# Performance work log

Measured on AMD Instinct MI355X. Metric: run time of the kernel, lower is better.

The kernel has to match this reference:

```python
import jax, jax.numpy as jnp
import numpy as np

N = 1_000_000
H, W = 480, 640
MIN_DEPTH, MAX_DEPTH = 0.0, 30.0


def setup_inputs() -> dict:
    key = jax.random.key(0)
    k1, k2, k3 = jax.random.split(key, 3)
    scale = jnp.array([W - 1, H - 1], dtype=jnp.float32)
    mkpts0_f = jax.random.uniform(k1, (N, 2), dtype=jnp.float32) * scale
    mkpts1_f = jax.random.uniform(k2, (N, 2), dtype=jnp.float32) * scale
    mconf = jax.random.uniform(k3, (N,), dtype=jnp.float32)
    K = jnp.array([[520.0, 0.0, 320.0],
                   [0.0, 520.0, 240.0],
                   [0.0, 0.0, 1.0]], dtype=jnp.float32)
    K0 = K[None]  # [1,3,3]
    K1 = K[None]
    c, s = float(np.cos(0.1)), float(np.sin(0.1))
    T_0to1 = jnp.array([[c, 0.0, s, 0.2],
                        [0.0, 1.0, 0.0, 0.0],
                        [-s, 0.0, c, 0.05],
                        [0.0, 0.0, 0.0, 1.0]], dtype=jnp.float32)[None]  # [1,4,4]
    image0 = jnp.zeros((1, 1, H, W), dtype=jnp.float32)
    m_bids = jnp.zeros((N,), dtype=jnp.int32)  # single batch element
    return {"T_0to1": T_0to1, "K0": K0, "K1": K1, "mconf": mconf,
            "mkpts0_f": mkpts0_f, "mkpts1_f": mkpts1_f,
            "image0": image0, "m_bids": m_bids}


def _triangulate(T_0to1, K0, K1, mconf, kpts0, kpts1):
    # Projection matrices: P0 = K0 @ [I|0], P1 = K1 @ T[:3,:]
    proj_identity = jnp.eye(3, 4, dtype=K0.dtype)
    P0 = K0[0] @ proj_identity          # [3,4]
    P1 = K1[0] @ T_0to1[0, :3, :]       # [3,4]
    P = jnp.stack([P0, P1], axis=0)     # [V=2,3,4]

    pts = jnp.stack([kpts0, kpts1], axis=1)              # [N,2,2]
    conf = jnp.stack([jnp.ones_like(mconf), mconf], 1)   # [N,2] (self conf = 1)

    # A[n,v] = pts[n,v,:,None] * P[v,2,None,:] - P[v,:2]   -> [N,V,2,4]
    A = pts[..., None] * P[None, :, 2, None, :] - P[None, :, :2, :]
    A = A * conf[:, :, None, None]
    A = A.reshape(A.shape[0], 4, 4)                       # [N,4,4]

    # torch.svd returns V with A = U S V^T; jnp gives Vh = V^T.
    _, _, Vh = jnp.linalg.svd(A)
    v = -Vh[:, 3, :]                                      # [N,4] = -V[:,:,3]
    points_3d = v[:, :3] / v[:, 3:4]                      # homogeneous -> euclidean
    # torch clamps to [-1000,1000] only when infs appear; the final depth value
    # after [0,30] clamp + filter is identical either way, so clip unconditionally.
    points_3d = jnp.clip(points_3d, -1000.0, 1000.0)

    z = jnp.clip(points_3d[:, 2], MIN_DEPTH, MAX_DEPTH)
    filt = (z > MIN_DEPTH) & (z < MAX_DEPTH)
    kp3d_val = z * filt.astype(z.dtype)
    return kp3d_val, points_3d


def reference(T_0to1, K0, K1, mconf, mkpts0_f, mkpts1_f, image0, m_bids):
    h, w = image0.shape[-2], image0.shape[-1]
    kp3d_val, _ = _triangulate(T_0to1, K0, K1, mconf, mkpts0_f, mkpts1_f)
    # generate_sparse_depth: depth[0, y, x] = kp3d_val (long() truncation)
    xi = mkpts0_f[:, 0].astype(jnp.int32)
    yi = mkpts0_f[:, 1].astype(jnp.int32)
    depth0_sparse = jnp.zeros((1, h, w), dtype=kp3d_val.dtype).at[0, yi, xi].set(kp3d_val)
    return depth0_sparse, kp3d_val
```

## Files before the change

### kernel.cpp

```cpp
#include <hip/hip_runtime.h>
#include <math.h>

#define N_PTS 1000000
#define H_IMG 480
#define W_IMG 640
#define PIX (H_IMG * W_IMG)
#define TPB 256
#define BPTS 1024
#define NBLK ((N_PTS + BPTS - 1) / BPTS)


__device__ __forceinline__ double frcp1(double b) {
  double r = __builtin_amdgcn_rcp(b);
  r = fma(fma(-b, r, 1.0), r, r);
  return r;
}
__device__ __forceinline__ double frcp2(double b) {
  double r = __builtin_amdgcn_rcp(b);
  r = fma(fma(-b, r, 1.0), r, r);
  r = fma(fma(-b, r, 1.0), r, r);
  return r;
}
__device__ __forceinline__ double fsqrt_pos(double x) {
  double r = __builtin_amdgcn_rsq(x);
  double y = x * r;
  return fma(0.5 * r, fma(-y, y, x), y);
}

#define ROT64(p, q)                                                            \
  do {                                                                         \
    double apq = Mv[p][q];                                                     \
    if (apq != 0.0) {                                                          \
      double app = Mv[p][p], aqq = Mv[q][q];                                   \
      double d = aqq - app;                                                    \
      double r = sqrt(fma(d, d, 4.0 * apq * apq));                             \
      double t = (2.0 * apq) / (d + copysign(r, d));                           \
      double c = rsqrt(fma(t, t, 1.0));                                        \
      double s = t * c;                                                        \
      Mv[p][p] = fma(-t, apq, app);                                            \
      Mv[q][q] = fma(t, apq, aqq);                                             \
      Mv[p][q] = 0.0;                                                          \
      Mv[q][p] = 0.0;                                                          \
      _Pragma("unroll") for (int k = 0; k < 4; k++) {                          \
        if (k != p && k != q) {                                                \
          double akp = Mv[k][p], akq = Mv[k][q];                               \
          double nkp = c * akp - s * akq;                                      \
          double nkq = s * akp + c * akq;                                      \
          Mv[k][p] = nkp; Mv[p][k] = nkp;                                      \
          Mv[k][q] = nkq; Mv[q][k] = nkq;                                      \
        }                                                                      \
      }                                                                        \
      { double v2p = Vr2[p], v2q = Vr2[q];                                     \
        Vr2[p] = c * v2p - s * v2q; Vr2[q] = s * v2p + c * v2q; }              \
      { double v3p = Vr3[p], v3q = Vr3[q];                                     \
        Vr3[p] = c * v3p - s * v3q; Vr3[q] = s * v3p + c * v3q; }              \
    }                                                                          \
  } while (0)

__device__ float tri_point_fp64(int n,
                                const float* __restrict__ T,
                                const float* __restrict__ K0,
                                const float* __restrict__ K1,
                                const float* __restrict__ mconf,
                                const float* __restrict__ kp0,
                                const float* __restrict__ kp1) {
  float2 p0 = ((const float2*)kp0)[n];
  float2 p1 = ((const float2*)kp1)[n];
  double conf = (double)mconf[n];
  double x0 = (double)p0.x, y0 = (double)p0.y;
  double x1 = (double)p1.x, y1 = (double)p1.y;

  double P0[3][4];
#pragma unroll
  for (int i = 0; i < 3; i++) {
#pragma unroll
    for (int j = 0; j < 3; j++) P0[i][j] = (double)K0[i * 3 + j];
    P0[i][3] = 0.0;
  }
  double P1[3][4];
#pragma unroll
  for (int i = 0; i < 3; i++) {
#pragma unroll
    for (int j = 0; j < 4; j++) {
      double s = 0.0;
#pragma unroll
      for (int k = 0; k < 3; k++)
        s += (double)K1[i * 3 + k] * (double)T[k * 4 + j];
      P1[i][j] = s;
    }
  }

  double Mv[4][4];
#pragma unroll
  for (int i = 0; i < 4; i++)
#pragma unroll
    for (int j = 0; j < 4; j++) Mv[i][j] = 0.0;

  double a[4];
#pragma unroll
  for (int j = 0; j < 4; j++) a[j] = x0 * P0[2][j] - P0[0][j];
#pragma unroll
  for (int i = 0; i < 4; i++)
#pragma unroll
    for (int j = 0; j < 4; j++) Mv[i][j] = fma(a[i], a[j], Mv[i][j]);
#pragma unroll
  for (int j = 0; j < 4; j++) a[j] = y0 * P0[2][j] - P0[1][j];
#pragma unroll
  for (int i = 0; i < 4; i++)
#pragma unroll
    for (int j = 0; j < 4; j++) Mv[i][j] = fma(a[i], a[j], Mv[i][j]);
#pragma unroll
  for (int j = 0; j < 4; j++) a[j] = conf * (x1 * P1[2][j] - P1[0][j]);
#pragma unroll
  for (int i = 0; i < 4; i++)
#pragma unroll
    for (int j = 0; j < 4; j++) Mv[i][j] = fma(a[i], a[j], Mv[i][j]);
#pragma unroll
  for (int j = 0; j < 4; j++) a[j] = conf * (y1 * P1[2][j] - P1[1][j]);
#pragma unroll
  for (int i = 0; i < 4; i++)
#pragma unroll
    for (int j = 0; j < 4; j++) Mv[i][j] = fma(a[i], a[j], Mv[i][j]);

  double Vr2[4] = {0.0, 0.0, 1.0, 0.0};
  double Vr3[4] = {0.0, 0.0, 0.0, 1.0};

  for (int sweep = 0; sweep < 4; sweep++) {
    ROT64(0, 1); ROT64(0, 2); ROT64(0, 3);
    ROT64(1, 2); ROT64(1, 3); ROT64(2, 3);
  }

  double e0 = Mv[0][0], e1 = Mv[1][1], e2 = Mv[2][2], e3 = Mv[3][3];
  bool b01 = e1 < e0;
  double ea = b01 ? e1 : e0;
  double za = b01 ? Vr2[1] : Vr2[0];
  double wa = b01 ? Vr3[1] : Vr3[0];
  bool b23 = e3 < e2;
  double eb = b23 ? e3 : e2;
  double zb = b23 ? Vr2[3] : Vr2[2];
  double wb = b23 ? Vr3[3] : Vr3[2];
  bool bf = eb < ea;
  double vz = bf ? zb : za;
  double vw = bf ? wb : wa;

  double z = vz / vw;
  z = fmin(fmax(z, 0.0), 30.0);
  bool filt = (z > 0.0) && (z < 30.0);
  return filt ? (float)z : 0.0f;
}

struct G10 { double m00, m01, m02, m03, m11, m12, m13, m22, m23, m33; };
struct P4 { double t1, t2, t3, t4; };
struct Adj10 { double a00, a01, a02, a03, a11, a12, a13, a22, a23, a33; };

__device__ __forceinline__ G10 gram(float2 p0, float2 p1, float conff,
                                    const double (&P0d)[3][4],
                                    const double (&P1d)[3][4]) {
  G10 g;
  g.m00 = g.m01 = g.m02 = g.m03 = g.m11 = 0.0;
  g.m12 = g.m13 = g.m22 = g.m23 = g.m33 = 0.0;
  double x0 = (double)p0.x, y0 = (double)p0.y;
  double x1 = (double)p1.x, y1 = (double)p1.y;
  double cf = (double)conff;
  double a[4];
#pragma unroll
  for (int rr = 0; rr < 4; rr++) {
    if (rr == 0) {
#pragma unroll
      for (int j = 0; j < 4; j++) a[j] = fma(x0, P0d[2][j], -P0d[0][j]);
    } else if (rr == 1) {
#pragma unroll
      for (int j = 0; j < 4; j++) a[j] = fma(y0, P0d[2][j], -P0d[1][j]);
    } else if (rr == 2) {
#pragma unroll
      for (int j = 0; j < 4; j++) a[j] = cf * fma(x1, P1d[2][j], -P1d[0][j]);
    } else {
#pragma unroll
      for (int j = 0; j < 4; j++) a[j] = cf * fma(y1, P1d[2][j], -P1d[1][j]);
    }
    g.m00 = fma(a[0], a[0], g.m00); g.m01 = fma(a[0], a[1], g.m01);
    g.m02 = fma(a[0], a[2], g.m02); g.m03 = fma(a[0], a[3], g.m03);
    g.m11 = fma(a[1], a[1], g.m11); g.m12 = fma(a[1], a[2], g.m12);
    g.m13 = fma(a[1], a[3], g.m13); g.m22 = fma(a[2], a[2], g.m22);
    g.m23 = fma(a[2], a[3], g.m23); g.m33 = fma(a[3], a[3], g.m33);
  }
  return g;
}

__device__ __forceinline__ P4 charpoly(const G10& m) {
  P4 p;
  p.t1 = (m.m00 + m.m11) + (m.m22 + m.m33);
  double ms0 = fma(m.m00, m.m11, -m.m01 * m.m01);
  double ms1 = fma(m.m00, m.m12, -m.m02 * m.m01);
  double ms2 = fma(m.m00, m.m13, -m.m03 * m.m01);
  double ms3 = fma(m.m01, m.m12, -m.m02 * m.m11);
  double ms4 = fma(m.m01, m.m13, -m.m03 * m.m11);
  double mc0 = fma(m.m02, m.m13, -m.m12 * m.m03);
  double mc1 = fma(m.m02, m.m23, -m.m22 * m.m03);
  double mc2 = fma(m.m02, m.m33, -m.m23 * m.m03);
  double mc3 = fma(m.m12, m.m23, -m.m22 * m.m13);
  double mc4 = fma(m.m12, m.m33, -m.m23 * m.m13);
  double mc5 = fma(m.m22, m.m33, -m.m23 * m.m23);
  double A00 = fma(m.m11, mc5, fma(-m.m12, mc4, m.m13 * mc3));
  double A01 = -fma(m.m01, mc5, fma(-m.m02, mc4, m.m03 * mc3));
  double A11 = fma(m.m00, mc5, fma(-m.m02, mc2, m.m03 * mc1));
  double A02 = fma(m.m01, mc4, fma(-m.m11, mc2, m.m13 * mc0));
  double A03 = -fma(m.m01, mc3, fma(-m.m11, mc1, m.m12 * mc0));
  double A22 = fma(m.m03, ms4, fma(-m.m13, ms2, m.m33 * ms0));
  double A33 = fma(m.m02, ms3, fma(-m.m12, ms1, m.m22 * ms0));
  p.t3 = (A00 + A11) + (A22 + A33);
  p.t4 = fma(m.m00, A00, fma(m.m01, A01, fma(m.m02, A02, m.m03 * A03)));
  double q02 = fma(m.m00, m.m22, -m.m02 * m.m02);
  double q03 = fma(m.m00, m.m33, -m.m03 * m.m03);
  double q12 = fma(m.m11, m.m22, -m.m12 * m.m12);
  double q13 = fma(m.m11, m.m33, -m.m13 * m.m13);
  p.t2 = ((ms0 + mc5) + (q02 + q03)) + (q12 + q13);
  return p;
}

__device__ __forceinline__ double lag_step(const P4& p, double mu,
                                           double t1_3, double t1_6,
                                           double t2_2) {
  double pv = fma(fma(fma(mu - p.t1, mu, p.t2), mu, -p.t3), mu, p.t4);
  double pd = fma(fma(fma(4.0, mu, -t1_3), mu, t2_2), mu, -p.t3);
  double pdd = fma(fma(12.0, mu, -t1_6), mu, t2_2);
  double rad = 3.0 * fma(3.0 * pd, pd, -4.0 * pv * pdd);
  double sq = fsqrt_pos(fmax(rad, 1e-300));
  double den = pd + copysign(sq, pd);
  return fma(-4.0 * pv, frcp1(den), mu);
}

__device__ __forceinline__ Adj10 adjugate(const G10& m, double mu) {
  double b00 = m.m00 - mu, b11 = m.m11 - mu;
  double b22 = m.m22 - mu, b33 = m.m33 - mu;
  double s0 = fma(b00, b11, -m.m01 * m.m01);
  double s1 = fma(b00, m.m12, -m.m02 * m.m01);
  double s2 = fma(b00, m.m13, -m.m03 * m.m01);
  double s3 = fma(m.m01, m.m12, -m.m02 * b11);
  double s4 = fma(m.m01, m.m13, -m.m03 * b11);
  double c0 = fma(m.m02, m.m13, -m.m12 * m.m03);
  double c1 = fma(m.m02, m.m23, -b22 * m.m03);
  double c2 = fma(m.m02, b33, -m.m23 * m.m03);
  double c3 = fma(m.m12, m.m23, -b22 * m.m13);
  double c4 = fma(m.m12, b33, -m.m23 * m.m13);
  double c5 = fma(b22, b33, -m.m23 * m.m23);
  Adj10 A;
  A.a00 = fma(b11, c5, fma(-m.m12, c4, m.m13 * c3));
  A.a01 = -fma(m.m01, c5, fma(-m.m02, c4, m.m03 * c3));
  A.a11 = fma(b00, c5, fma(-m.m02, c2, m.m03 * c1));
  A.a02 = fma(m.m01, c4, fma(-b11, c2, m.m13 * c0));
  A.a12 = -fma(b00, c4, fma(-m.m01, c2, m.m03 * c0));
  A.a22 = fma(m.m03, s4, fma(-m.m13, s2, b33 * s0));
  A.a03 = -fma(m.m01, c3, fma(-b11, c1, m.m12 * c0));
  A.a13 = fma(b00, c3, fma(-m.m01, c1, m.m02 * c0));
  A.a23 = -fma(m.m03, s3, fma(-m.m13, s1, m.m23 * s0));
  A.a33 = fma(m.m02, s3, fma(-m.m12, s1, b22 * s0));
  return A;
}

__device__ __forceinline__ void finish(const Adj10& A, double* z_out,
                                       bool* ok_out) {
  double w10 = A.a00, w11 = A.a01, w12 = A.a02, w13 = A.a03;
  double bd = fabs(A.a00);
  { double d1 = fabs(A.a11);
    bool c = d1 > bd;
    w10 = c ? A.a01 : w10; w11 = c ? A.a11 : w11;
    w12 = c ? A.a12 : w12; w13 = c ? A.a13 : w13; bd = c ? d1 : bd; }
  { double d2 = fabs(A.a22);
    bool c = d2 > bd;
    w10 = c ? A.a02 : w10; w11 = c ? A.a12 : w11;
    w12 = c ? A.a22 : w12; w13 = c ? A.a23 : w13; bd = c ? d2 : bd; }
  { double d3 = fabs(A.a33);
    bool c = d3 > bd;
    w10 = c ? A.a03 : w10; w11 = c ? A.a13 : w11;
    w12 = c ? A.a23 : w12; w13 = c ? A.a33 : w13; }

  double u0 = fma(A.a00, w10, fma(A.a01, w11, fma(A.a02, w12, A.a03 * w13)));
  double u1 = fma(A.a01, w10, fma(A.a11, w11, fma(A.a12, w12, A.a13 * w13)));
  double u2 = fma(A.a02, w10, fma(A.a12, w11, fma(A.a22, w12, A.a23 * w13)));
  double u3 = fma(A.a03, w10, fma(A.a13, w11, fma(A.a23, w12, A.a33 * w13)));
  double v2 = fma(A.a02, u0, fma(A.a12, u1, fma(A.a22, u2, A.a23 * u3)));
  double v3 = fma(A.a03, u0, fma(A.a13, u1, fma(A.a23, u2, A.a33 * u3)));

  double z3 = v2 * frcp2(v3);

  double cross = fabs(fma(v2, u3, -(u2 * v3)));
  double rhs = 1e-3 * fmax(fabs(v3 * u3), fabs(v2 * u3));
  *ok_out = (cross < rhs) && (fabs(z3 - 30.0) > 0.1);
  *z_out = z3;
}

__global__ __launch_bounds__(TPB, 2) void tri_main(
    const float* __restrict__ T,
    const float* __restrict__ K0,
    const float* __restrict__ K1,
    const float* __restrict__ mconf,
    const float* __restrict__ kp0,
    const float* __restrict__ kp1,
    float* __restrict__ out_kp3d,
    unsigned long long* __restrict__ ws_pix)
{
  __shared__ unsigned short s_list[BPTS];
  __shared__ int s_cnt;

  int tid = threadIdx.x;
  int base = blockIdx.x * BPTS;
  if (tid == 0) s_cnt = 0;
  __syncthreads();

  double P0d[3][4], P1d[3][4];
#pragma unroll
  for (int i = 0; i < 3; i++) {
#pragma unroll
    for (int j = 0; j < 3; j++) P0d[i][j] = (double)K0[i * 3 + j];
    P0d[i][3] = 0.0;
  }
#pragma unroll
  for (int i = 0; i < 3; i++) {
#pragma unroll
    for (int j = 0; j < 4; j++) {
      double s = 0.0;
#pragma unroll
      for (int k = 0; k < 3; k++)
        s += (double)K1[i * 3 + k] * (double)T[k * 4 + j];
      P1d[i][j] = s;
    }
  }

#pragma unroll 1
  for (int r = 0; r < BPTS / (2 * TPB); r++) {
    int l0 = r * (2 * TPB) + tid;
    int l1 = l0 + TPB;
    int n0 = base + l0;
    int n1 = base + l1;
    bool act0 = n0 < N_PTS;
    bool act1 = n1 < N_PTS;
    int nc0 = act0 ? n0 : (N_PTS - 1);
    int nc1 = act1 ? n1 : (N_PTS - 1);

    float2 p0a = ((const float2*)kp0)[nc0];
    float2 p1a = ((const float2*)kp1)[nc0];
    float cfa = mconf[nc0];
    float2 p0b = ((const float2*)kp0)[nc1];
    float2 p1b = ((const float2*)kp1)[nc1];
    float cfb = mconf[nc1];

    G10 gA = gram(p0a, p1a, cfa, P0d, P1d);
    G10 gB = gram(p0b, p1b, cfb, P0d, P1d);
    P4 cA = charpoly(gA);
    P4 cB = charpoly(gB);
    double muA = cA.t4 * frcp1(cA.t3);
    double muB = cB.t4 * frcp1(cB.t3);
    double t1_3A = 3.0 * cA.t1, t1_6A = 6.0 * cA.t1, t2_2A = 2.0 * cA.t2;
    double t1_3B = 3.0 * cB.t1, t1_6B = 6.0 * cB.t1, t2_2B = 2.0 * cB.t2;
#pragma unroll
    for (int it = 0; it < 3; it++) {
      muA = lag_step(cA, muA, t1_3A, t1_6A, t2_2A);
      muB = lag_step(cB, muB, t1_3B, t1_6B, t2_2B);
    }
    Adj10 aA = adjugate(gA, muA);
    Adj10 aB = adjugate(gB, muB);
    double zA, zB;
    bool okA, okB;
    finish(aA, &zA, &okA);
    finish(aB, &zB, &okB);

    if (act0) {
      if (okA) {
        double zc = fmin(fmax(zA, 0.0), 30.0);
        bool filt = (zc > 0.0) && (zc < 30.0);
        float kp = filt ? (float)zc : 0.0f;
        out_kp3d[n0] = kp;
        int pix = (int)p0a.y * W_IMG + (int)p0a.x;
        atomicMax(&ws_pix[pix],
                  ((unsigned long long)(0xC0000000u | (unsigned)n0) << 32) |
                      (unsigned long long)__float_as_uint(kp));
      } else {
        int idx = atomicAdd(&s_cnt, 1);
        s_list[idx] = (unsigned short)l0;
      }
    }
    if (act1) {
      if (okB) {
        double zc = fmin(fmax(zB, 0.0), 30.0);
        bool filt = (zc > 0.0) && (zc < 30.0);
        float kp = filt ? (float)zc : 0.0f;
        out_kp3d[n1] = kp;
        int pix = (int)p0b.y * W_IMG + (int)p0b.x;
        atomicMax(&ws_pix[pix],
                  ((unsigned long long)(0xC0000000u | (unsigned)n1) << 32) |
                      (unsigned long long)__float_as_uint(kp));
      } else {
        int idx = atomicAdd(&s_cnt, 1);
        s_list[idx] = (unsigned short)l1;
      }
    }
  }

  __syncthreads();

  int cnt = s_cnt;
  for (int i = tid; i < cnt; i += TPB) {
    int n = base + (int)s_list[i];
    float kp = tri_point_fp64(n, T, K0, K1, mconf, kp0, kp1);
    out_kp3d[n] = kp;
    float2 p0 = ((const float2*)kp0)[n];
    int pix = (int)p0.y * W_IMG + (int)p0.x;
    atomicMax(&ws_pix[pix],
              ((unsigned long long)(0xC0000000u | (unsigned)n) << 32) |
                  (unsigned long long)__float_as_uint(kp));
  }
}

__global__ __launch_bounds__(TPB) void unpack_depth(
    const unsigned long long* __restrict__ ws_pix,
    float* __restrict__ out_depth)
{
  int p = blockIdx.x * blockDim.x + threadIdx.x;
  if (p < PIX) {
    unsigned long long v = ws_pix[p];
    unsigned int hi = (unsigned int)(v >> 32);
    out_depth[p] =
        (hi >= 0xC0000000u) ? __uint_as_float((unsigned int)v) : 0.0f;
  }
}

extern "C" void kernel_launch(void* const* d_in, const int* in_sizes, int n_in,
                              void* d_out, int out_size, void* d_ws, size_t ws_size,
                              hipStream_t stream) {
  const float* T     = (const float*)d_in[0];
  const float* K0    = (const float*)d_in[1];
  const float* K1    = (const float*)d_in[2];
  const float* mconf = (const float*)d_in[3];
  const float* kp0   = (const float*)d_in[4];
  const float* kp1   = (const float*)d_in[5];

  float* out = (float*)d_out;
  unsigned long long* ws_pix = (unsigned long long*)d_ws;

  tri_main<<<NBLK, TPB, 0, stream>>>(T, K0, K1, mconf, kp0, kp1,
                                     out + PIX, ws_pix);

  unpack_depth<<<(PIX + TPB - 1) / TPB, TPB, 0, stream>>>(ws_pix, out);
}
```

Baseline: 126.4 us.

## Replicate depth scatter workspace per XCD and reduce planes in unpack

Each XCD now writes its packed depth atomicMax results into its own plane of the workspace, selected via the hardware XCC_ID register, using workgroup-scope relaxed atomics. The unpack kernel then takes the max across all 8 planes. This aims to avoid cross-die atomic traffic and coherence costs on the shared depth map. In exchange, the unpack pass reads eight times more workspace, and correctness depends on the narrower atomic scope still being resolved at L2.

```diff
diff --git a/kernel.cpp b/kernel.cpp
--- a/kernel.cpp
+++ b/kernel.cpp
@@ -8,6 +8,7 @@
 #define TPB 256
 #define BPTS 1024
 #define NBLK ((N_PTS + BPTS - 1) / BPTS)
+#define NXCD 8
 
 
 __device__ __forceinline__ double frcp1(double b) {
@@ -25,6 +26,12 @@
   double r = __builtin_amdgcn_rsq(x);
   double y = x * r;
   return fma(0.5 * r, fma(-y, y, x), y);
+}
+
+__device__ __forceinline__ unsigned xcc_id() {
+  unsigned x;
+  asm volatile("s_getreg_b32 %0, hwreg(HW_REG_XCC_ID)" : "=s"(x));
+  return x & (NXCD - 1);
 }
 
 #define ROT64(p, q)                                                            \
@@ -290,6 +297,19 @@
   *z_out = z3;
 }
 
+template <int NREP>
+__device__ __forceinline__ void scatter(unsigned long long* ws_pix,
+                                        unsigned plane, int pix,
+                                        unsigned long long key) {
+  if (NREP == 8) {
+    __hip_atomic_fetch_max(&ws_pix[(size_t)plane * PIX + pix], key,
+                           __ATOMIC_RELAXED, __HIP_MEMORY_SCOPE_WORKGROUP);
+  } else {
+    atomicMax(&ws_pix[pix], key);
+  }
+}
+
+template <int NREP>
 __global__ __launch_bounds__(TPB, 2) void tri_main(
     const float* __restrict__ T,
     const float* __restrict__ K0,
@@ -308,6 +328,8 @@
   if (tid == 0) s_cnt = 0;
   __syncthreads();
 
+  unsigned plane = (NREP == 8) ? xcc_id() : 0;
+
   double P0d[3][4], P1d[3][4];
 #pragma unroll
   for (int i = 0; i < 3; i++) {
@@ -372,9 +394,9 @@
         float kp = filt ? (float)zc : 0.0f;
         out_kp3d[n0] = kp;
         int pix = (int)p0a.y * W_IMG + (int)p0a.x;
-        atomicMax(&ws_pix[pix],
-                  ((unsigned long long)(0xC0000000u | (unsigned)n0) << 32) |
-                      (unsigned long long)__float_as_uint(kp));
+        scatter<NREP>(ws_pix, plane, pix,
+                      ((unsigned long long)(0xC0000000u | (unsigned)n0) << 32) |
+                          (unsigned long long)__float_as_uint(kp));
       } else {
         int idx = atomicAdd(&s_cnt, 1);
         s_list[idx] = (unsigned short)l0;
@@ -387,9 +409,9 @@
         float kp = filt ? (float)zc : 0.0f;
         out_kp3d[n1] = kp;
         int pix = (int)p0b.y * W_IMG + (int)p0b.x;
-        atomicMax(&ws_pix[pix],
-                  ((unsigned long long)(0xC0000000u | (unsigned)n1) << 32) |
-                      (unsigned long long)__float_as_uint(kp));
+        scatter<NREP>(ws_pix, plane, pix,
+                      ((unsigned long long)(0xC0000000u | (unsigned)n1) << 32) |
+                          (unsigned long long)__float_as_uint(kp));
       } else {
         int idx = atomicAdd(&s_cnt, 1);
         s_list[idx] = (unsigned short)l1;
@@ -406,22 +428,28 @@
     out_kp3d[n] = kp;
     float2 p0 = ((const float2*)kp0)[n];
     int pix = (int)p0.y * W_IMG + (int)p0.x;
-    atomicMax(&ws_pix[pix],
-              ((unsigned long long)(0xC0000000u | (unsigned)n) << 32) |
-                  (unsigned long long)__float_as_uint(kp));
-  }
-}
-
+    scatter<NREP>(ws_pix, plane, pix,
+                  ((unsigned long long)(0xC0000000u | (unsigned)n) << 32) |
+                      (unsigned long long)__float_as_uint(kp));
+  }
+}
+
+template <int NREP>
 __global__ __launch_bounds__(TPB) void unpack_depth(
     const unsigned long long* __restrict__ ws_pix,
     float* __restrict__ out_depth)
 {
   int p = blockIdx.x * blockDim.x + threadIdx.x;
   if (p < PIX) {
-    unsigned long long v = ws_pix[p];
-    unsigned int hi = (unsigned int)(v >> 32);
+    unsigned long long best = ws_pix[p];
+#pragma unroll
+    for (int r = 1; r < NREP; r++) {
+      unsigned long long v = ws_pix[(size_t)r * PIX + p];
+      best = (v > best) ? v : best;
+    }
+    unsigned int hi = (unsigned int)(best >> 32);
     out_depth[p] =
-        (hi >= 0xC0000000u) ? __uint_as_float((unsigned int)v) : 0.0f;
+        (hi >= 0xC0000000u) ? __uint_as_float((unsigned int)best) : 0.0f;
   }
 }
 
@@ -438,8 +466,14 @@
   float* out = (float*)d_out;
   unsigned long long* ws_pix = (unsigned long long*)d_ws;
 
-  tri_main<<<NBLK, TPB, 0, stream>>>(T, K0, K1, mconf, kp0, kp1,
-                                     out + PIX, ws_pix);
-
-  unpack_depth<<<(PIX + TPB - 1) / TPB, TPB, 0, stream>>>(ws_pix, out);
-}
+  bool rep = ws_size >= (size_t)NXCD * PIX * 8;
+  if (rep) {
+    tri_main<8><<<NBLK, TPB, 0, stream>>>(T, K0, K1, mconf, kp0, kp1,
+                                          out + PIX, ws_pix);
+    unpack_depth<8><<<(PIX + TPB - 1) / TPB, TPB, 0, stream>>>(ws_pix, out);
+  } else {
+    tri_main<1><<<NBLK, TPB, 0, stream>>>(T, K0, K1, mconf, kp0, kp1,
+                                          out + PIX, ws_pix);
+    unpack_depth<1><<<(PIX + TPB - 1) / TPB, TPB, 0, stream>>>(ws_pix, out);
+  }
+}
```

New measurement: 131.1 us. +3.7%, slower.
